# Kernel optimization log

Hardware: AMD Instinct MI355X
Metric: run time of the kernel (lower is better)

## Reference

```python
import jax, jax.numpy as jnp
import numpy as np
from jax import lax

B, N, W, L, H = 8, 1024, 1024, 12, 16
EPS = 1e-5


def setup_inputs() -> dict:
    key = jax.random.key(0)
    ks = jax.random.split(key, 14)
    std = 0.25 / np.sqrt(W)  # init_scale * sqrt(1/width)
    inp = {
        "x": jax.random.normal(ks[0], (B, N, W), dtype=jnp.float32),
        # stacked per-layer params, leading dim L
        "ln1_g": jnp.ones((L, W), jnp.float32),
        "ln1_b": jnp.zeros((L, W), jnp.float32),
        "w_qkv": jax.random.normal(ks[1], (L, W, 3 * W), jnp.float32) * std,
        "b_qkv": jnp.zeros((L, 3 * W), jnp.float32),
        "w_o":   jax.random.normal(ks[2], (L, W, W), jnp.float32) * std,
        "b_o":   jnp.zeros((L, W), jnp.float32),
        "ln2_g": jnp.ones((L, W), jnp.float32),
        "ln2_b": jnp.zeros((L, W), jnp.float32),
        "w_fc":  jax.random.normal(ks[3], (L, W, 4 * W), jnp.float32) * std,
        "b_fc":  jnp.zeros((L, 4 * W), jnp.float32),
        "w_pr":  jax.random.normal(ks[4], (L, 4 * W, W), jnp.float32) * std,
        "b_pr":  jnp.zeros((L, W), jnp.float32),
    }
    return inp


def _layernorm(x, g, b):
    mu = jnp.mean(x, axis=-1, keepdims=True)
    var = jnp.mean(jnp.square(x - mu), axis=-1, keepdims=True)
    return (x - mu) * lax.rsqrt(var + EPS) * g + b


def _attention(qkv, heads):
    # qkv: [B, N, 3W]; matches QKVMultiheadAttention exactly
    bs, n_ctx, width3 = qkv.shape
    attn_ch = width3 // heads // 3
    scale = 1.0 / np.sqrt(np.sqrt(attn_ch))
    qkv = qkv.reshape(bs, n_ctx, heads, 3 * attn_ch)
    q, k, v = jnp.split(qkv, 3, axis=-1)  # each [B,N,H,c]
    w = jnp.einsum("bthc,bshc->bhts", q * scale, k * scale)
    w = jax.nn.softmax(w.astype(jnp.float32), axis=-1).astype(qkv.dtype)
    out = jnp.einsum("bhts,bshc->bthc", w, v)
    return out.reshape(bs, n_ctx, heads * attn_ch)


def reference(x, ln1_g, ln1_b, w_qkv, b_qkv, w_o, b_o,
              ln2_g, ln2_b, w_fc, b_fc, w_pr, b_pr):
    params = (ln1_g, ln1_b, w_qkv, b_qkv, w_o, b_o,
              ln2_g, ln2_b, w_fc, b_fc, w_pr, b_pr)

    def step(h, p):
        (g1, bb1, wqkv, bqkv, wo, bo, g2, bb2, wfc, bfc, wpr, bpr) = p
        a = _layernorm(h, g1, bb1)
        a = jnp.einsum("bnw,wk->bnk", a, wqkv) + bqkv
        a = _attention(a, H)
        a = jnp.einsum("bnw,wk->bnk", a, wo) + bo
        h = h + a
        m = _layernorm(h, g2, bb2)
        m = jax.nn.gelu(jnp.einsum("bnw,wf->bnf", m, wfc) + bfc, approximate=False)
        m = jnp.einsum("bnf,fw->bnw", m, wpr) + bpr
        return h + m, None

    out, _ = lax.scan(step, x, params)
    return out
```

## Files before the change

### kernel.cpp

```cpp
#include <hip/hip_runtime.h>
#include <cstdint>
#include <cstddef>

#define WDIM 1024
#define BDIM 8
#define NDIM 1024
#define LDIM 12
#define HDIM 16
#define MROWS (BDIM * NDIM)

using bf16x8 = __attribute__((ext_vector_type(8))) __bf16;
using f32x4  = __attribute__((ext_vector_type(4))) float;
using u32x4  = __attribute__((ext_vector_type(4))) uint32_t;
using u16x8  = __attribute__((ext_vector_type(8))) ushort;

static __device__ __forceinline__ f32x4 mfma16(bf16x8 a, bf16x8 b, f32x4 c) {
  return __builtin_amdgcn_mfma_f32_16x16x32_bf16(a, b, c, 0, 0, 0);
}

static __device__ __forceinline__ ushort f2bf(float f) {
  uint32_t u = __builtin_bit_cast(uint32_t, f);
  u = (u + 0x7FFFu + ((u >> 16) & 1u)) >> 16;
  return (ushort)u;
}

static __device__ __forceinline__ uint32_t cvtpk(float lo, float hi) {
  uint32_t r;
  asm("v_cvt_pk_bf16_f32 %0, %1, %2" : "=v"(r) : "v"(lo), "v"(hi));
  return r;
}

static __device__ __forceinline__ void g2lds16(const void* g, void* l) {
  __builtin_amdgcn_global_load_lds(
      (__attribute__((address_space(1))) void*)(g),
      (__attribute__((address_space(3))) void*)(l), 16, 0, 0);
}

__global__ __launch_bounds__(256) void ln_kernel(const float* __restrict__ h,
                                                 const float* __restrict__ g,
                                                 const float* __restrict__ b,
                                                 ushort* __restrict__ out) {
  const int w = threadIdx.x >> 6, l = threadIdx.x & 63;
  const int row = blockIdx.x * 4 + w;
  const float4* rp = (const float4*)(h + (size_t)row * WDIM);
  float4 v[4];
  float s = 0.f, s2 = 0.f;
  #pragma unroll
  for (int j = 0; j < 4; ++j) {
    v[j] = rp[j * 64 + l];
    s  += v[j].x + v[j].y + v[j].z + v[j].w;
    s2 += v[j].x * v[j].x + v[j].y * v[j].y + v[j].z * v[j].z + v[j].w * v[j].w;
  }
  #pragma unroll
  for (int off = 32; off; off >>= 1) {
    s  += __shfl_xor(s, off);
    s2 += __shfl_xor(s2, off);
  }
  const float mu   = s * (1.0f / WDIM);
  const float var  = s2 * (1.0f / WDIM) - mu * mu;
  const float rstd = rsqrtf(var + 1e-5f);
  ushort4* op = (ushort4*)(out + (size_t)row * WDIM);
  #pragma unroll
  for (int j = 0; j < 4; ++j) {
    const float4 gv = ((const float4*)g)[j * 64 + l];
    const float4 bv = ((const float4*)b)[j * 64 + l];
    ushort4 o;
    o.x = f2bf((v[j].x - mu) * rstd * gv.x + bv.x);
    o.y = f2bf((v[j].y - mu) * rstd * gv.y + bv.y);
    o.z = f2bf((v[j].z - mu) * rstd * gv.z + bv.z);
    o.w = f2bf((v[j].w - mu) * rstd * gv.w + bv.w);
    op[j * 64 + l] = o;
  }
}

__global__ __launch_bounds__(256) void transpose_cvt(const float* __restrict__ in,
                                                     ushort* __restrict__ out,
                                                     int K, int N) {
  __shared__ float sm[64][65];
  const int n0 = blockIdx.x * 64, k0 = blockIdx.y * 64;
  const int t = threadIdx.x;
  const int lk = t >> 4;
  const int ln4 = (t & 15) * 4;
  #pragma unroll
  for (int j = 0; j < 4; ++j) {
    const float4 v = *(const float4*)&in[(size_t)(k0 + j * 16 + lk) * N + n0 + ln4];
    sm[j * 16 + lk][ln4 + 0] = v.x;
    sm[j * 16 + lk][ln4 + 1] = v.y;
    sm[j * 16 + lk][ln4 + 2] = v.z;
    sm[j * 16 + lk][ln4 + 3] = v.w;
  }
  __syncthreads();
  const int n  = t >> 2;
  const int ks = (t & 3) * 16;
  ushort tmp[16];
  #pragma unroll
  for (int j = 0; j < 16; ++j) tmp[j] = f2bf(sm[ks + j][n]);
  ushort* op = &out[(size_t)(n0 + n) * K + k0 + ks];
  *(uint4*)&op[0] = *(const uint4*)&tmp[0];
  *(uint4*)&op[8] = *(const uint4*)&tmp[8];
}

__global__ __launch_bounds__(256) void v_transpose(const ushort* __restrict__ qkv,
                                                   ushort* __restrict__ vT) {
  const int nb = blockIdx.x, bh = blockIdx.y;
  const int b = bh >> 4, h = bh & 15;
  const int tid = threadIdx.x;
  __shared__ ushort smT[64 * 64];
  const int n0 = nb * 64;
  const size_t rowb = (size_t)b * NDIM;
  #pragma unroll
  for (int p = 0; p < 2; ++p) {
    const int n  = p * 32 + (tid >> 3);
    const int d0 = (tid & 7) * 8;
    const uint4 vv = *(const uint4*)(qkv + (rowb + n0 + n) * 3072 + h * 192 + 128 + d0);
    const ushort* e = (const ushort*)&vv;
    const int key = d0;
    #pragma unroll
    for (int j = 0; j < 8; ++j)
      smT[(d0 + j) * 64 + (n ^ key)] = e[j];
  }
  __syncthreads();
  #pragma unroll
  for (int p = 0; p < 2; ++p) {
    const int d  = p * 32 + (tid >> 3);
    const int nc = (tid & 7) * 8;
    const int key = (d >> 3) << 3;
    const uint4 ov = *(const uint4*)&smT[d * 64 + (nc ^ key)];
    *(uint4*)(vT + ((size_t)bh * 64 + d) * NDIM + n0 + nc) = ov;
  }
}

enum { EPI_BF16 = 0, EPI_GELU = 2 };

template <int EPI>
__global__ __launch_bounds__(512, 2) void gemm256_kernel(
    const ushort* __restrict__ A, const ushort* __restrict__ Bt,
    const float* __restrict__ bias, ushort* __restrict__ outb,
    int M, int N, int K) {
  __shared__ ushort smA[2 * 2 * 256 * 32];
  __shared__ ushort smB[2 * 2 * 256 * 32];
  const int tid = threadIdx.x;
  const int w = tid >> 6, l = tid & 63;
  const int lr = l & 15, lg = l >> 4;
  const int wm = w >> 2, wn = w & 3;

  const int gx = gridDim.x;
  const int nwg = gx * gridDim.y;
  const int id0 = blockIdx.y * gx + blockIdx.x;
  const int id = (id0 & 7) * (nwg >> 3) + (id0 >> 3);
  const int row0 = (id / gx) * 256, col0 = (id % gx) * 256;

  const int KT = K >> 6;
  const int srow_l = l >> 2;
  const int scol = (((l & 3) ^ ((l >> 3) & 3)) * 8);
  const int ks = ((lg ^ ((lr >> 1) & 3)) * 8);

  f32x4 acc[8][4] = {};

  auto stageA = [&](int tau, int hh) {
    const int base = (((tau & 1) * 2 + hh) * 8192);
    const int colb = tau * 64 + hh * 32 + scol;
    #pragma unroll
    for (int j = 0; j < 2; ++j) {
      const int c = j * 8 + w;
      g2lds16(A + (size_t)(row0 + 16 * c + srow_l) * K + colb, &smA[base + c * 512]);
    }
  };
  auto stageB = [&](int tau, int hh) {
    const int base = (((tau & 1) * 2 + hh) * 8192);
    const int colb = tau * 64 + hh * 32 + scol;
    #pragma unroll
    for (int j = 0; j < 2; ++j) {
      const int c = j * 8 + w;
      g2lds16(Bt + (size_t)(col0 + 16 * c + srow_l) * K + colb, &smB[base + c * 512]);
    }
  };

  stageA(0, 0); stageB(0, 0);
  stageA(0, 1); stageB(0, 1);
  stageA(1, 0); stageB(1, 0);
  asm volatile("s_waitcnt vmcnt(8)" ::: "memory");
  __builtin_amdgcn_sched_barrier(0);
  __builtin_amdgcn_s_barrier();

  for (int tau = 0; tau < KT; ++tau) {
    const int ab0 = (tau & 1) * 16384;
    const int ab1 = ab0 + 8192;
    bf16x8 af[8], bf0, bf1;

    #pragma unroll
    for (int m = 0; m < 8; ++m)
      af[m] = *(const bf16x8*)&smA[ab0 + (wm * 128 + m * 16 + lr) * 32 + ks];
    bf0 = *(const bf16x8*)&smB[ab0 + (wn * 64 + lr) * 32 + ks];
    bf1 = *(const bf16x8*)&smB[ab0 + (wn * 64 + 16 + lr) * 32 + ks];
    if (tau + 1 < KT) stageA(tau + 1, 1);
    __builtin_amdgcn_s_barrier();
    asm volatile("s_waitcnt lgkmcnt(0)" ::: "memory");
    __builtin_amdgcn_sched_barrier(0);
    __builtin_amdgcn_s_setprio(1);
    #pragma unroll
    for (int m = 0; m < 8; ++m) {
      acc[m][0] = mfma16(af[m], bf0, acc[m][0]);
      acc[m][1] = mfma16(af[m], bf1, acc[m][1]);
    }
    __builtin_amdgcn_s_setprio(0);
    __builtin_amdgcn_s_barrier();

    bf0 = *(const bf16x8*)&smB[ab0 + (wn * 64 + 32 + lr) * 32 + ks];
    bf1 = *(const bf16x8*)&smB[ab0 + (wn * 64 + 48 + lr) * 32 + ks];
    if (tau + 1 < KT) stageB(tau + 1, 1);
    __builtin_amdgcn_s_barrier();
    asm volatile("s_waitcnt lgkmcnt(0)" ::: "memory");
    __builtin_amdgcn_sched_barrier(0);
    __builtin_amdgcn_s_setprio(1);
    #pragma unroll
    for (int m = 0; m < 8; ++m) {
      acc[m][2] = mfma16(af[m], bf0, acc[m][2]);
      acc[m][3] = mfma16(af[m], bf1, acc[m][3]);
    }
    __builtin_amdgcn_s_setprio(0);
    if (tau + 1 < KT) { asm volatile("s_waitcnt vmcnt(8)" ::: "memory"); }
    else              { asm volatile("s_waitcnt vmcnt(0)" ::: "memory"); }
    __builtin_amdgcn_sched_barrier(0);
    __builtin_amdgcn_s_barrier();

    #pragma unroll
    for (int m = 0; m < 8; ++m)
      af[m] = *(const bf16x8*)&smA[ab1 + (wm * 128 + m * 16 + lr) * 32 + ks];
    bf0 = *(const bf16x8*)&smB[ab1 + (wn * 64 + lr) * 32 + ks];
    bf1 = *(const bf16x8*)&smB[ab1 + (wn * 64 + 16 + lr) * 32 + ks];
    if (tau + 2 < KT) { stageA(tau + 2, 0); stageB(tau + 2, 0); }
    __builtin_amdgcn_s_barrier();
    asm volatile("s_waitcnt lgkmcnt(0)" ::: "memory");
    __builtin_amdgcn_sched_barrier(0);
    __builtin_amdgcn_s_setprio(1);
    #pragma unroll
    for (int m = 0; m < 8; ++m) {
      acc[m][0] = mfma16(af[m], bf0, acc[m][0]);
      acc[m][1] = mfma16(af[m], bf1, acc[m][1]);
    }
    __builtin_amdgcn_s_setprio(0);
    __builtin_amdgcn_s_barrier();

    bf0 = *(const bf16x8*)&smB[ab1 + (wn * 64 + 32 + lr) * 32 + ks];
    bf1 = *(const bf16x8*)&smB[ab1 + (wn * 64 + 48 + lr) * 32 + ks];
    __builtin_amdgcn_s_barrier();
    asm volatile("s_waitcnt lgkmcnt(0)" ::: "memory");
    __builtin_amdgcn_sched_barrier(0);
    __builtin_amdgcn_s_setprio(1);
    #pragma unroll
    for (int m = 0; m < 8; ++m) {
      acc[m][2] = mfma16(af[m], bf0, acc[m][2]);
      acc[m][3] = mfma16(af[m], bf1, acc[m][3]);
    }
    __builtin_amdgcn_s_setprio(0);
    if (tau + 2 < KT)      { asm volatile("s_waitcnt vmcnt(8)" ::: "memory"); }
    else if (tau + 1 < KT) { asm volatile("s_waitcnt vmcnt(4)" ::: "memory"); }
    __builtin_amdgcn_sched_barrier(0);
    __builtin_amdgcn_s_barrier();
  }

  #pragma unroll
  for (int m = 0; m < 8; ++m) {
    #pragma unroll
    for (int n = 0; n < 4; ++n) {
      #pragma unroll
      for (int i = 0; i < 4; ++i) {
        const int r = row0 + wm * 128 + m * 16 + lg * 4 + i;
        const int c = col0 + wn * 64 + n * 16 + lr;
        float v = acc[m][n][i] + bias[c];
        if constexpr (EPI == EPI_GELU) {
          v = 0.5f * v * (1.0f + erff(v * 0.70710678118f));
        }
        outb[(size_t)r * N + c] = f2bf(v);
      }
    }
  }
}

enum { GEPI_BF16 = 0, GEPI_RES = 1 };

template <int EPI>
__global__ __launch_bounds__(256) void gemm_kernel(
    const ushort* __restrict__ A, const ushort* __restrict__ Bt,
    const float* __restrict__ bias, float* __restrict__ resid,
    ushort* __restrict__ outb, int M, int N, int K) {
  __shared__ ushort smA[2][128 * 64];
  __shared__ ushort smB[2][128 * 64];
  const int tid = threadIdx.x;
  const int w = tid >> 6, l = tid & 63;
  const int lr = l & 15, lg = l >> 4;
  const int wr = (w >> 1) * 64, wc = (w & 1) * 64;

  const int gx = gridDim.x;
  const int nwg = gx * gridDim.y;
  const int id0 = blockIdx.y * gx + blockIdx.x;
  const int id = (id0 & 7) * (nwg >> 3) + (id0 >> 3);
  const int row0 = (id / gx) * 128, col0 = (id % gx) * 128;

  const int srow = tid >> 3;
  const int sslot = tid & 7;
  f32x4 acc[4][4] = {};
  const int KT = K >> 6;

  auto stage = [&](int buf, int kt) {
    const int kb = kt << 6;
    #pragma unroll
    for (int j = 0; j < 4; ++j) {
      const int r = j * 32 + srow;
      const int sc = ((sslot ^ (r & 7)) * 8);
      g2lds16(A  + (size_t)(row0 + r) * K + kb + sc, &smA[buf][j * 2048 + w * 512]);
      g2lds16(Bt + (size_t)(col0 + r) * K + kb + sc, &smB[buf][j * 2048 + w * 512]);
    }
  };

  stage(0, 0);
  int cur = 0;
  for (int kt = 0; kt < KT; ++kt) {
    __syncthreads();
    if (kt + 1 < KT) stage(cur ^ 1, kt + 1);
    bf16x8 af[2][4], bfr[2][4];
    const int rs = lr & 7;
    #pragma unroll
    for (int kk = 0; kk < 2; ++kk) {
      #pragma unroll
      for (int t = 0; t < 4; ++t) {
        const int k8 = (kk * 4 + lg) ^ rs;
        af[kk][t]  = *(const bf16x8*)&smA[cur][(wr + t * 16 + lr) * 64 + k8 * 8];
        bfr[kk][t] = *(const bf16x8*)&smB[cur][(wc + t * 16 + lr) * 64 + k8 * 8];
      }
    }
    __builtin_amdgcn_s_setprio(1);
    #pragma unroll
    for (int kk = 0; kk < 2; ++kk)
      #pragma unroll
      for (int mt = 0; mt < 4; ++mt)
        #pragma unroll
        for (int nt = 0; nt < 4; ++nt)
          acc[mt][nt] = mfma16(af[kk][mt], bfr[kk][nt], acc[mt][nt]);
    __builtin_amdgcn_s_setprio(0);
    cur ^= 1;
  }

  #pragma unroll
  for (int mt = 0; mt < 4; ++mt) {
    #pragma unroll
    for (int nt = 0; nt < 4; ++nt) {
      #pragma unroll
      for (int i = 0; i < 4; ++i) {
        const int r = row0 + wr + mt * 16 + lg * 4 + i;
        const int c = col0 + wc + nt * 16 + lr;
        float v = acc[mt][nt][i] + bias[c];
        if constexpr (EPI == GEPI_RES) {
          resid[(size_t)r * N + c] += v;
        } else {
          outb[(size_t)r * N + c] = f2bf(v);
        }
      }
    }
  }
}

__global__ __launch_bounds__(512) void attn_kernel(const ushort* __restrict__ qkv,
                                                   const ushort* __restrict__ vT,
                                                   ushort* __restrict__ out) {
  const int qb = blockIdx.x;
  const int bh = blockIdx.y;
  const int b = bh >> 4, h = bh & 15;
  const int tid = threadIdx.x;
  const int w = tid >> 6, l = tid & 63;
  const int lr = l & 15, lg = l >> 4;
  __shared__ ushort smK[2][64 * 64];
  __shared__ ushort smV[2][64 * 64];
  const int q0 = qb * 128 + w * 16;
  const size_t rowb = (size_t)b * NDIM;
  const ushort* vhead = vT + (size_t)bh * 64 * NDIM;

  const u16x8 ob = {0x3F80, 0x3F80, 0x3F80, 0x3F80, 0x3F80, 0x3F80, 0x3F80, 0x3F80};
  const bf16x8 onesv = __builtin_bit_cast(bf16x8, ob);

  const int srow = l >> 3;
  const int skey = (srow & 3) ^ ((w & 1) << 2);
  const int scol = ((l & 7) ^ skey) * 8;
  const ushort* kg = qkv + (rowb + w * 8 + srow) * 3072 + h * 192 + 64 + scol;
  const ushort* vg = vhead + (size_t)(w * 8 + srow) * NDIM + scol;

  auto stage = [&](int buf, int kb) {
    g2lds16(kg + (size_t)kb * 64 * 3072, &smK[buf][w * 512]);
    g2lds16(vg + kb * 64,                &smV[buf][w * 512]);
  };

  bf16x8 qf0, qf1;
  {
    const ushort* qp = qkv + (rowb + q0 + lr) * 3072 + h * 192;
    qf0 = *(const bf16x8*)(qp + lg * 8);
    qf1 = *(const bf16x8*)(qp + 32 + lg * 8);
  }
  f32x4 o[4] = {};
  f32x4 lacc = {0.f, 0.f, 0.f, 0.f};

  const int rbase = (lr >> 2) * 8 + (lr & 3);
  const int kkey  = (lr & 3) ^ (((lr >> 2) & 1) << 2);
  const int vkey  = (lr & 3) ^ (((lr >> 3) & 1) << 2);
  const int kp0 = (lg ^ kkey) * 8, kp1 = ((4 + lg) ^ kkey) * 8;
  const int vp0 = (lg ^ vkey) * 8, vp1 = ((4 + lg) ^ vkey) * 8;

  stage(0, 0);
  int cur = 0;
  for (int kb = 0; kb < NDIM / 64; ++kb) {
    __syncthreads();
    if (kb + 1 < NDIM / 64) stage(cur ^ 1, kb + 1);

    f32x4 s[2][2];
    __builtin_amdgcn_s_setprio(1);
    #pragma unroll
    for (int hh = 0; hh < 2; ++hh) {
      #pragma unroll
      for (int m = 0; m < 2; ++m) {
        const int r = hh * 32 + rbase + 4 * m;
        const ushort* kr = &smK[cur][r * 64];
        const bf16x8 kf0 = *(const bf16x8*)&kr[kp0];
        const bf16x8 kf1 = *(const bf16x8*)&kr[kp1];
        f32x4 z = {0.f, 0.f, 0.f, 0.f};
        s[hh][m] = mfma16(kf1, qf1, mfma16(kf0, qf0, z));
      }
    }
    __builtin_amdgcn_s_setprio(0);

    bf16x8 pf[2];
    #pragma unroll
    for (int hh = 0; hh < 2; ++hh) {
      u32x4 pk;
      pk[0] = cvtpk(__expf(s[hh][0][0] * 0.125f), __expf(s[hh][0][1] * 0.125f));
      pk[1] = cvtpk(__expf(s[hh][0][2] * 0.125f), __expf(s[hh][0][3] * 0.125f));
      pk[2] = cvtpk(__expf(s[hh][1][0] * 0.125f), __expf(s[hh][1][1] * 0.125f));
      pk[3] = cvtpk(__expf(s[hh][1][2] * 0.125f), __expf(s[hh][1][3] * 0.125f));
      pf[hh] = __builtin_bit_cast(bf16x8, pk);
    }

    __builtin_amdgcn_s_setprio(1);
    lacc = mfma16(pf[0], onesv, mfma16(pf[1], onesv, lacc));
    #pragma unroll
    for (int dt = 0; dt < 4; ++dt) {
      const ushort* vrow = &smV[cur][(dt * 16 + lr) * 64];
      const bf16x8 vf0 = *(const bf16x8*)&vrow[vp0];
      const bf16x8 vf1 = *(const bf16x8*)&vrow[vp1];
      o[dt] = mfma16(pf[0], vf0, mfma16(pf[1], vf1, o[dt]));
    }
    __builtin_amdgcn_s_setprio(0);
    cur ^= 1;
  }

  #pragma unroll
  for (int i = 0; i < 4; ++i) {
    const float inv = 1.0f / lacc[i];
    const size_t orow = (rowb + q0 + lg * 4 + i) * (size_t)WDIM;
    #pragma unroll
    for (int dt = 0; dt < 4; ++dt)
      out[orow + h * 64 + dt * 16 + lr] = f2bf(o[dt][i] * inv);
  }
}

extern "C" void kernel_launch(void* const* d_in, const int* in_sizes, int n_in,
                              void* d_out, int out_size, void* d_ws, size_t ws_size,
                              hipStream_t stream) {
  const float* x     = (const float*)d_in[0];
  const float* ln1_g = (const float*)d_in[1];
  const float* ln1_b = (const float*)d_in[2];
  const float* w_qkv = (const float*)d_in[3];
  const float* b_qkv = (const float*)d_in[4];
  const float* w_o   = (const float*)d_in[5];
  const float* b_o   = (const float*)d_in[6];
  const float* ln2_g = (const float*)d_in[7];
  const float* ln2_b = (const float*)d_in[8];
  const float* w_fc  = (const float*)d_in[9];
  const float* b_fc  = (const float*)d_in[10];
  const float* w_pr  = (const float*)d_in[11];
  const float* b_pr  = (const float*)d_in[12];

  float* hbuf = (float*)d_out;

  uint8_t* p = (uint8_t*)d_ws;
  ushort* wqkv_t = (ushort*)p; p += (size_t)3072 * 1024 * 2;
  ushort* wo_t   = (ushort*)p; p += (size_t)1024 * 1024 * 2;
  ushort* wfc_t  = (ushort*)p; p += (size_t)4096 * 1024 * 2;
  ushort* wpr_t  = (ushort*)p; p += (size_t)1024 * 4096 * 2;
  ushort* lnb    = (ushort*)p; p += (size_t)MROWS * 1024 * 2;
  ushort* qkvb   = (ushort*)p; p += (size_t)MROWS * 3072 * 2;
  ushort* attnb  = (ushort*)p; p += (size_t)MROWS * 1024 * 2;
  ushort* mlpb   = (ushort*)p; p += (size_t)MROWS * 4096 * 2;
  ushort* vTb    = (ushort*)p; p += (size_t)BDIM * HDIM * 64 * NDIM * 2;

  hipMemcpyAsync(hbuf, x, (size_t)MROWS * WDIM * sizeof(float),
                 hipMemcpyDeviceToDevice, stream);

  for (int l = 0; l < LDIM; ++l) {
    ln_kernel<<<MROWS / 4, 256, 0, stream>>>(hbuf, ln1_g + l * 1024, ln1_b + l * 1024, lnb);
    transpose_cvt<<<dim3(48, 16), 256, 0, stream>>>(
        w_qkv + (size_t)l * 1024 * 3072, wqkv_t, 1024, 3072);
    gemm256_kernel<EPI_BF16><<<dim3(12, 32), 512, 0, stream>>>(
        lnb, wqkv_t, b_qkv + (size_t)l * 3072, qkvb, MROWS, 3072, 1024);
    v_transpose<<<dim3(16, 128), 256, 0, stream>>>(qkvb, vTb);
    attn_kernel<<<dim3(8, 128), 512, 0, stream>>>(qkvb, vTb, attnb);
    transpose_cvt<<<dim3(16, 16), 256, 0, stream>>>(
        w_o + (size_t)l * 1024 * 1024, wo_t, 1024, 1024);
    gemm_kernel<GEPI_RES><<<dim3(8, 64), 256, 0, stream>>>(
        attnb, wo_t, b_o + (size_t)l * 1024, hbuf, nullptr, MROWS, 1024, 1024);
    ln_kernel<<<MROWS / 4, 256, 0, stream>>>(hbuf, ln2_g + l * 1024, ln2_b + l * 1024, lnb);
    transpose_cvt<<<dim3(64, 16), 256, 0, stream>>>(
        w_fc + (size_t)l * 1024 * 4096, wfc_t, 1024, 4096);
    gemm256_kernel<EPI_GELU><<<dim3(16, 32), 512, 0, stream>>>(
        lnb, wfc_t, b_fc + (size_t)l * 4096, mlpb, MROWS, 4096, 1024);
    transpose_cvt<<<dim3(16, 64), 256, 0, stream>>>(
        w_pr + (size_t)l * 4096 * 1024, wpr_t, 4096, 1024);
    gemm_kernel<GEPI_RES><<<dim3(8, 64), 256, 0, stream>>>(
        mlpb, wpr_t, b_pr + (size_t)l * 1024, hbuf, nullptr, MROWS, 1024, 4096);
  }
}
```

Measured before the change: 4.419 ms.

## Replace 128x128 residual GEMM with pipelined 256x128 tile kernel

The 128x128 residual-add GEMM used for the attention output and MLP projection is replaced by a 512-thread 256x128 tile kernel. It splits each 64-wide K step into two 32-wide halves and interleaves global-to-LDS staging with MFMA phases, using explicit barriers and vmcnt/lgkmcnt waits. The larger tile increases operand reuse per workgroup and hides load latency better. In exchange the grid shrinks to 256 workgroups (one wave of CUs on MI355X) and the hand-written wait counts are fragile.

New measurement: 4.816 ms. 9.0% more time.

```diff
diff --git a/kernel.cpp b/kernel.cpp
--- a/kernel.cpp
+++ b/kernel.cpp
@@ -278,84 +278,128 @@
   }
 }
 
-enum { GEPI_BF16 = 0, GEPI_RES = 1 };
-
-template <int EPI>
-__global__ __launch_bounds__(256) void gemm_kernel(
+__global__ __launch_bounds__(512, 1) void gemm256x128_kernel(
     const ushort* __restrict__ A, const ushort* __restrict__ Bt,
     const float* __restrict__ bias, float* __restrict__ resid,
-    ushort* __restrict__ outb, int M, int N, int K) {
-  __shared__ ushort smA[2][128 * 64];
-  __shared__ ushort smB[2][128 * 64];
+    int M, int N, int K) {
+  __shared__ ushort smA[2 * 2 * 256 * 32];
+  __shared__ ushort smB[2 * 2 * 128 * 32];
   const int tid = threadIdx.x;
   const int w = tid >> 6, l = tid & 63;
   const int lr = l & 15, lg = l >> 4;
-  const int wr = (w >> 1) * 64, wc = (w & 1) * 64;
+  const int wm = w >> 2, wn = w & 3;
 
   const int gx = gridDim.x;
   const int nwg = gx * gridDim.y;
   const int id0 = blockIdx.y * gx + blockIdx.x;
   const int id = (id0 & 7) * (nwg >> 3) + (id0 >> 3);
-  const int row0 = (id / gx) * 128, col0 = (id % gx) * 128;
-
-  const int srow = tid >> 3;
-  const int sslot = tid & 7;
-  f32x4 acc[4][4] = {};
+  const int row0 = (id / gx) * 256, col0 = (id % gx) * 128;
+
   const int KT = K >> 6;
-
-  auto stage = [&](int buf, int kt) {
-    const int kb = kt << 6;
-    #pragma unroll
-    for (int j = 0; j < 4; ++j) {
-      const int r = j * 32 + srow;
-      const int sc = ((sslot ^ (r & 7)) * 8);
-      g2lds16(A  + (size_t)(row0 + r) * K + kb + sc, &smA[buf][j * 2048 + w * 512]);
-      g2lds16(Bt + (size_t)(col0 + r) * K + kb + sc, &smB[buf][j * 2048 + w * 512]);
+  const int srow_l = l >> 2;
+  const int scol = (((l & 3) ^ ((l >> 3) & 3)) * 8);
+  const int ks = ((lg ^ ((lr >> 1) & 3)) * 8);
+
+  f32x4 acc[8][2] = {};
+
+  auto stageA = [&](int tau, int hh) {
+    const int base = (((tau & 1) * 2 + hh) * 8192);
+    const int colb = tau * 64 + hh * 32 + scol;
+    #pragma unroll
+    for (int j = 0; j < 2; ++j) {
+      const int c = j * 8 + w;
+      g2lds16(A + (size_t)(row0 + 16 * c + srow_l) * K + colb, &smA[base + c * 512]);
     }
   };
-
-  stage(0, 0);
-  int cur = 0;
-  for (int kt = 0; kt < KT; ++kt) {
-    __syncthreads();
-    if (kt + 1 < KT) stage(cur ^ 1, kt + 1);
-    bf16x8 af[2][4], bfr[2][4];
-    const int rs = lr & 7;
-    #pragma unroll
-    for (int kk = 0; kk < 2; ++kk) {
-      #pragma unroll
-      for (int t = 0; t < 4; ++t) {
-        const int k8 = (kk * 4 + lg) ^ rs;
-        af[kk][t]  = *(const bf16x8*)&smA[cur][(wr + t * 16 + lr) * 64 + k8 * 8];
-        bfr[kk][t] = *(const bf16x8*)&smB[cur][(wc + t * 16 + lr) * 64 + k8 * 8];
-      }
-    }
-    __builtin_amdgcn_s_setprio(1);
-    #pragma unroll
-    for (int kk = 0; kk < 2; ++kk)
-      #pragma unroll
-      for (int mt = 0; mt < 4; ++mt)
-        #pragma unroll
-        for (int nt = 0; nt < 4; ++nt)
-          acc[mt][nt] = mfma16(af[kk][mt], bfr[kk][nt], acc[mt][nt]);
-    __builtin_amdgcn_s_setprio(0);
-    cur ^= 1;
-  }
-
-  #pragma unroll
-  for (int mt = 0; mt < 4; ++mt) {
-    #pragma unroll
-    for (int nt = 0; nt < 4; ++nt) {
+  auto stageB = [&](int tau, int hh) {
+    const int base = (((tau & 1) * 2 + hh) * 4096);
+    const int colb = tau * 64 + hh * 32 + scol;
+    g2lds16(Bt + (size_t)(col0 + 16 * w + srow_l) * K + colb, &smB[base + w * 512]);
+  };
+
+  stageA(0, 0); stageB(0, 0);
+  stageA(0, 1); stageB(0, 1);
+  stageA(1, 0); stageB(1, 0);
+  asm volatile("s_waitcnt vmcnt(6)" ::: "memory");
+  __builtin_amdgcn_sched_barrier(0);
+  __builtin_amdgcn_s_barrier();
+
+  for (int tau = 0; tau < KT; ++tau) {
+    const int aab0 = (tau & 1) * 16384;
+    const int aab1 = aab0 + 8192;
+    const int bab0 = (tau & 1) * 8192;
+    const int bab1 = bab0 + 4096;
+    bf16x8 af[8], bf0, bf1;
+
+    #pragma unroll
+    for (int m = 0; m < 8; ++m)
+      af[m] = *(const bf16x8*)&smA[aab0 + (wm * 128 + m * 16 + lr) * 32 + ks];
+    bf0 = *(const bf16x8*)&smB[bab0 + (wn * 32 + lr) * 32 + ks];
+    if (tau + 1 < KT) stageA(tau + 1, 1);
+    __builtin_amdgcn_s_barrier();
+    asm volatile("s_waitcnt lgkmcnt(0)" ::: "memory");
+    __builtin_amdgcn_sched_barrier(0);
+    __builtin_amdgcn_s_setprio(1);
+    #pragma unroll
+    for (int m = 0; m < 8; ++m)
+      acc[m][0] = mfma16(af[m], bf0, acc[m][0]);
+    __builtin_amdgcn_s_setprio(0);
+    __builtin_amdgcn_s_barrier();
+
+    bf1 = *(const bf16x8*)&smB[bab0 + (wn * 32 + 16 + lr) * 32 + ks];
+    if (tau + 1 < KT) stageB(tau + 1, 1);
+    __builtin_amdgcn_s_barrier();
+    asm volatile("s_waitcnt lgkmcnt(0)" ::: "memory");
+    __builtin_amdgcn_sched_barrier(0);
+    __builtin_amdgcn_s_setprio(1);
+    #pragma unroll
+    for (int m = 0; m < 8; ++m)
+      acc[m][1] = mfma16(af[m], bf1, acc[m][1]);
+    __builtin_amdgcn_s_setprio(0);
+    if (tau + 1 < KT) { asm volatile("s_waitcnt vmcnt(6)" ::: "memory"); }
+    else              { asm volatile("s_waitcnt vmcnt(0)" ::: "memory"); }
+    __builtin_amdgcn_sched_barrier(0);
+    __builtin_amdgcn_s_barrier();
+
+    #pragma unroll
+    for (int m = 0; m < 8; ++m)
+      af[m] = *(const bf16x8*)&smA[aab1 + (wm * 128 + m * 16 + lr) * 32 + ks];
+    bf0 = *(const bf16x8*)&smB[bab1 + (wn * 32 + lr) * 32 + ks];
+    if (tau + 2 < KT) { stageA(tau + 2, 0); stageB(tau + 2, 0); }
+    __builtin_amdgcn_s_barrier();
+    asm volatile("s_waitcnt lgkmcnt(0)" ::: "memory");
+    __builtin_amdgcn_sched_barrier(0);
+    __builtin_amdgcn_s_setprio(1);
+    #pragma unroll
+    for (int m = 0; m < 8; ++m)
+      acc[m][0] = mfma16(af[m], bf0, acc[m][0]);
+    __builtin_amdgcn_s_setprio(0);
+    __builtin_amdgcn_s_barrier();
+
+    bf1 = *(const bf16x8*)&smB[bab1 + (wn * 32 + 16 + lr) * 32 + ks];
+    __builtin_amdgcn_s_barrier();
+    asm volatile("s_waitcnt lgkmcnt(0)" ::: "memory");
+    __builtin_amdgcn_sched_barrier(0);
+    __builtin_amdgcn_s_setprio(1);
+    #pragma unroll
+    for (int m = 0; m < 8; ++m)
+      acc[m][1] = mfma16(af[m], bf1, acc[m][1]);
+    __builtin_amdgcn_s_setprio(0);
+    if (tau + 2 < KT)      { asm volatile("s_waitcnt vmcnt(6)" ::: "memory"); }
+    else if (tau + 1 < KT) { asm volatile("s_waitcnt vmcnt(3)" ::: "memory"); }
+    __builtin_amdgcn_sched_barrier(0);
+    __builtin_amdgcn_s_barrier();
+  }
+
+  #pragma unroll
+  for (int m = 0; m < 8; ++m) {
+    #pragma unroll
+    for (int n = 0; n < 2; ++n) {
       #pragma unroll
       for (int i = 0; i < 4; ++i) {
-        const int r = row0 + wr + mt * 16 + lg * 4 + i;
-        const int c = col0 + wc + nt * 16 + lr;
-        float v = acc[mt][nt][i] + bias[c];
-        if constexpr (EPI == GEPI_RES) {
-          resid[(size_t)r * N + c] += v;
-        } else {
-          outb[(size_t)r * N + c] = f2bf(v);
-        }
+        const int r = row0 + wm * 128 + m * 16 + lg * 4 + i;
+        const int c = col0 + wn * 32 + n * 16 + lr;
+        resid[(size_t)r * N + c] += acc[m][n][i] + bias[c];
       }
     }
   }
@@ -504,8 +548,8 @@
     attn_kernel<<<dim3(8, 128), 512, 0, stream>>>(qkvb, vTb, attnb);
     transpose_cvt<<<dim3(16, 16), 256, 0, stream>>>(
         w_o + (size_t)l * 1024 * 1024, wo_t, 1024, 1024);
-    gemm_kernel<GEPI_RES><<<dim3(8, 64), 256, 0, stream>>>(
-        attnb, wo_t, b_o + (size_t)l * 1024, hbuf, nullptr, MROWS, 1024, 1024);
+    gemm256x128_kernel<<<dim3(8, 32), 512, 0, stream>>>(
+        attnb, wo_t, b_o + (size_t)l * 1024, hbuf, MROWS, 1024, 1024);
     ln_kernel<<<MROWS / 4, 256, 0, stream>>>(hbuf, ln2_g + l * 1024, ln2_b + l * 1024, lnb);
     transpose_cvt<<<dim3(64, 16), 256, 0, stream>>>(
         w_fc + (size_t)l * 1024 * 4096, wfc_t, 1024, 4096);
@@ -513,7 +557,7 @@
         lnb, wfc_t, b_fc + (size_t)l * 4096, mlpb, MROWS, 4096, 1024);
     transpose_cvt<<<dim3(16, 64), 256, 0, stream>>>(
         w_pr + (size_t)l * 4096 * 1024, wpr_t, 4096, 1024);
-    gemm_kernel<GEPI_RES><<<dim3(8, 64), 256, 0, stream>>>(
-        mlpb, wpr_t, b_pr + (size_t)l * 1024, hbuf, nullptr, MROWS, 1024, 4096);
-  }
-}
+    gemm256x128_kernel<<<dim3(8, 32), 512, 0, stream>>>(
+        mlpb, wpr_t, b_pr + (size_t)l * 1024, hbuf, MROWS, 1024, 4096);
+  }
+}
```
